# Performance work log

Hardware: AMD Instinct MI355X
Metric: run time of the kernel (lower is better)

Reference implementation:

```python
import math
import jax, jax.numpy as jnp
import numpy as np


def _shapley_tables(L):
    """Static subset-lattice tables for L views.

    masks: [M, L] 0/1 membership of view l in subset m (M = 2^L).
    coef:  [L, M] Shapley combination coefficients so that
           shapley[l] = sum_m coef[l, m] * relu(Linear(sum_{j in m} feats[j])).
    Derivation (faithful to the torch loops): for view i and every nonempty
    subset S not containing i, contrib = f(sum_{S u {i}}) - f(feats_i) with
    weight |S|! (L-|S|-1)! / L!, plus f(feats_i)/L.  Letting T = S u {i}
    (|T| >= 2, i in T) and noting sum of weights over all S is (L-1)/L and
    f(feats_i) = f(sum over singleton {i}):
      coef[i, T]          = (|T|-1)! (L-|T|)! / L!   for |T|>=2, i in T
      coef[i, {i}]       += -(L-1)/L + 1/L = -(L-2)/L
    """
    M = 1 << L
    fact = math.factorial
    masks = np.zeros((M, L), np.float32)
    coef = np.zeros((L, M), np.float32)
    for m in range(M):
        bits = [i for i in range(L) if (m >> i) & 1]
        for i in bits:
            masks[m, i] = 1.0
        t = len(bits)
        if t >= 2:
            wgt = fact(t - 1) * fact(L - t) / fact(L)
            for i in bits:
                coef[i, m] += wgt
    for i in range(L):
        coef[i, 1 << i] += -(L - 2) / L
    return jnp.asarray(masks), jnp.asarray(coef)


def setup_inputs() -> dict:
    key = jax.random.key(0)
    k1, k2 = jax.random.split(key)
    L, C, H, W = 5, 64, 128, 256
    feats = jax.random.normal(k1, (L, C, H, W), dtype=jnp.float32)
    w = jax.random.normal(k2, (C, 1), dtype=jnp.float32) / np.sqrt(C)
    b = jnp.zeros((1,), dtype=jnp.float32)
    return {"feats": feats, "w": w, "b": b}


def reference(feats, w, b):
    L, C, H, W = feats.shape
    N = H * W
    masks, coef = _shapley_tables(L)
    x = feats.reshape(L, C, N).transpose(0, 2, 1)          # [L, N, C]
    # all 2^L subset sums in one GEMM over the (tiny) L axis
    subset_sums = jnp.einsum('ml,lnc->mnc', masks, x)       # [M, N, C]
    f_sums = jax.nn.relu(subset_sums @ w + b)               # [M, N, 1]
    shapley = jnp.einsum('lm,mnj->lnj', coef, f_sums)       # [L, N, 1]
    attn = jax.nn.softmax(shapley, axis=0)                  # softmax over views
    fused = jnp.sum(x * attn, axis=0)                       # [N, C]
    return fused.T.reshape(C, H, W)
```

## Files before the change

### kernel.cpp

```cpp
#include <hip/hip_runtime.h>


constexpr int L_VIEWS = 5;
constexpr int C_CH    = 64;
constexpr int NPIX    = 128 * 256;

typedef float floatx4 __attribute__((ext_vector_type(4)));

__global__ __launch_bounds__(256, 4)
void shapley_fusion_kernel(const float* __restrict__ feats,
                           const float* __restrict__ w,
                           const float* __restrict__ bptr,
                           float* __restrict__ out)
{
    const int tid  = threadIdx.x;
    const int h    = tid >> 6;
    const int lane = tid & 63;
    const int q    = lane & 7;
    const int g    = (lane >> 3) & 7;
    const int win  = blockIdx.x * 32;
    const int nq   = win + q * 4;
    const int cA   = h * 8 + g;
    const int cB   = cA + 32;

    const float w0   = w[cA];
    const float w1   = w[cB];
    const float bias = bptr[0];

    float4 va[L_VIEWS][2];
#pragma unroll
    for (int l = 0; l < L_VIEWS; ++l) {
        va[l][0] = *reinterpret_cast<const float4*>(
            feats + ((size_t)(l * C_CH + cA) * NPIX + nq));
        va[l][1] = *reinterpret_cast<const float4*>(
            feats + ((size_t)(l * C_CH + cB) * NPIX + nq));
    }

    float d[L_VIEWS][4];
#pragma unroll
    for (int l = 0; l < L_VIEWS; ++l) {
        d[l][0] = va[l][0].x * w0 + va[l][1].x * w1;
        d[l][1] = va[l][0].y * w0 + va[l][1].y * w1;
        d[l][2] = va[l][0].z * w0 + va[l][1].z * w1;
        d[l][3] = va[l][0].w * w0 + va[l][1].w * w1;
    }

#pragma unroll
    for (int l = 0; l < L_VIEWS; ++l) {
#pragma unroll
        for (int j = 0; j < 4; ++j) {
            d[l][j] += __shfl_xor(d[l][j], 8, 64);
            d[l][j] += __shfl_xor(d[l][j], 16, 64);
            d[l][j] += __shfl_xor(d[l][j], 32, 64);
        }
    }

    __shared__ float4 xl[4][8][L_VIEWS];
    if (g == 0) {
#pragma unroll
        for (int l = 0; l < L_VIEWS; ++l) {
            float4 t; t.x = d[l][0]; t.y = d[l][1]; t.z = d[l][2]; t.w = d[l][3];
            xl[h][q][l] = t;
        }
    }
    __syncthreads();

    const int jm = g & 3;
    const float* xf = reinterpret_cast<const float*>(xl);
    float dm[L_VIEWS];
#pragma unroll
    for (int l = 0; l < L_VIEWS; ++l) {
        float s = 0.f;
#pragma unroll
        for (int hh = 0; hh < 4; ++hh)
            s += xf[(((hh * 8 + q) * L_VIEWS) + l) * 4 + jm];
        dm[l] = s;
    }

    constexpr float WTS[6] = {0.f, -0.6f, 0.05f, 1.0f / 30.0f, 0.05f, 0.2f};

    float S = bias;
    float sh[L_VIEWS] = {0.f, 0.f, 0.f, 0.f, 0.f};
#pragma unroll
    for (int t = 1; t < 32; ++t) {
        const int gm   = t ^ (t >> 1);
        const int bit  = __builtin_ctz(t);
        const bool add = (gm >> bit) & 1;
        S = add ? (S + dm[bit]) : (S - dm[bit]);
        const float f  = fmaxf(S, 0.f);
        const float wt = WTS[__builtin_popcount(gm)];
#pragma unroll
        for (int i = 0; i < L_VIEWS; ++i)
            if (gm & (1 << i)) sh[i] += wt * f;
    }

    float mx = sh[0];
#pragma unroll
    for (int i = 1; i < L_VIEWS; ++i) mx = fmaxf(mx, sh[i]);
    float e[L_VIEWS];
    float sum = 0.f;
#pragma unroll
    for (int i = 0; i < L_VIEWS; ++i) { e[i] = __expf(sh[i] - mx); sum += e[i]; }
    const float inv = 1.f / sum;
    float attn_mine[L_VIEWS];
#pragma unroll
    for (int i = 0; i < L_VIEWS; ++i) attn_mine[i] = e[i] * inv;

    float attn[L_VIEWS][4];
#pragma unroll
    for (int l = 0; l < L_VIEWS; ++l)
#pragma unroll
        for (int j = 0; j < 4; ++j)
            attn[l][j] = __shfl(attn_mine[l], q + 8 * j, 64);

#pragma unroll
    for (int k = 0; k < 2; ++k) {
        const int c = (k == 0) ? cA : cB;
        floatx4 acc;
        acc.x = va[0][k].x * attn[0][0];
        acc.y = va[0][k].y * attn[0][1];
        acc.z = va[0][k].z * attn[0][2];
        acc.w = va[0][k].w * attn[0][3];
#pragma unroll
        for (int l = 1; l < L_VIEWS; ++l) {
            acc.x += va[l][k].x * attn[l][0];
            acc.y += va[l][k].y * attn[l][1];
            acc.z += va[l][k].z * attn[l][2];
            acc.w += va[l][k].w * attn[l][3];
        }
        __builtin_nontemporal_store(acc,
            reinterpret_cast<floatx4*>(out + (size_t)c * NPIX + nq));
    }
}

extern "C" void kernel_launch(void* const* d_in, const int* in_sizes, int n_in,
                              void* d_out, int out_size, void* d_ws, size_t ws_size,
                              hipStream_t stream) {
    const float* feats = (const float*)d_in[0];
    const float* w     = (const float*)d_in[1];
    const float* b     = (const float*)d_in[2];
    float* out         = (float*)d_out;

    shapley_fusion_kernel<<<NPIX / 32, 256, 0, stream>>>(feats, w, b, out);
}
```

Before: 15.59 us.

## Process two pixel windows per block and use DPP for xor-8 reduction

Each block now handles two 32-pixel windows. Both windows' feature loads are issued up front, so twice the memory traffic is in flight per thread before any compute starts. The first butterfly step of the channel reduction becomes a DPP row operation instead of a ds_swizzle/shuffle. The launch-bounds occupancy hint is dropped and the grid is halved. The cost is doubled register pressure for the loaded data, plus lower occupancy and fewer blocks.

```diff
diff --git a/kernel.cpp b/kernel.cpp
--- a/kernel.cpp
+++ b/kernel.cpp
@@ -7,65 +7,50 @@
 
 typedef float floatx4 __attribute__((ext_vector_type(4)));
 
-__global__ __launch_bounds__(256, 4)
-void shapley_fusion_kernel(const float* __restrict__ feats,
-                           const float* __restrict__ w,
-                           const float* __restrict__ bptr,
-                           float* __restrict__ out)
+__device__ __forceinline__ float xor8_add_dpp(float x) {
+    int y = __builtin_amdgcn_update_dpp(0, __float_as_int(x),
+                                        0x128 , 0xF, 0xF, true);
+    return x + __int_as_float(y);
+}
+
+struct Ctx {
+    int q, g, h, jm, cA, cB;
+    float w0, w1, bias;
+};
+
+__device__ __forceinline__ void window_compute(
+    const Ctx& cx, const float4 (&va)[L_VIEWS][2], int nq,
+    float4 (*xl)[8][L_VIEWS],
+    float* __restrict__ out)
 {
-    const int tid  = threadIdx.x;
-    const int h    = tid >> 6;
-    const int lane = tid & 63;
-    const int q    = lane & 7;
-    const int g    = (lane >> 3) & 7;
-    const int win  = blockIdx.x * 32;
-    const int nq   = win + q * 4;
-    const int cA   = h * 8 + g;
-    const int cB   = cA + 32;
-
-    const float w0   = w[cA];
-    const float w1   = w[cB];
-    const float bias = bptr[0];
-
-    float4 va[L_VIEWS][2];
-#pragma unroll
-    for (int l = 0; l < L_VIEWS; ++l) {
-        va[l][0] = *reinterpret_cast<const float4*>(
-            feats + ((size_t)(l * C_CH + cA) * NPIX + nq));
-        va[l][1] = *reinterpret_cast<const float4*>(
-            feats + ((size_t)(l * C_CH + cB) * NPIX + nq));
-    }
-
     float d[L_VIEWS][4];
 #pragma unroll
     for (int l = 0; l < L_VIEWS; ++l) {
-        d[l][0] = va[l][0].x * w0 + va[l][1].x * w1;
-        d[l][1] = va[l][0].y * w0 + va[l][1].y * w1;
-        d[l][2] = va[l][0].z * w0 + va[l][1].z * w1;
-        d[l][3] = va[l][0].w * w0 + va[l][1].w * w1;
+        d[l][0] = va[l][0].x * cx.w0 + va[l][1].x * cx.w1;
+        d[l][1] = va[l][0].y * cx.w0 + va[l][1].y * cx.w1;
+        d[l][2] = va[l][0].z * cx.w0 + va[l][1].z * cx.w1;
+        d[l][3] = va[l][0].w * cx.w0 + va[l][1].w * cx.w1;
     }
 
 #pragma unroll
     for (int l = 0; l < L_VIEWS; ++l) {
 #pragma unroll
         for (int j = 0; j < 4; ++j) {
-            d[l][j] += __shfl_xor(d[l][j], 8, 64);
+            d[l][j] = xor8_add_dpp(d[l][j]);
             d[l][j] += __shfl_xor(d[l][j], 16, 64);
             d[l][j] += __shfl_xor(d[l][j], 32, 64);
         }
     }
 
-    __shared__ float4 xl[4][8][L_VIEWS];
-    if (g == 0) {
+    if (cx.g == 0) {
 #pragma unroll
         for (int l = 0; l < L_VIEWS; ++l) {
             float4 t; t.x = d[l][0]; t.y = d[l][1]; t.z = d[l][2]; t.w = d[l][3];
-            xl[h][q][l] = t;
+            xl[cx.h][cx.q][l] = t;
         }
     }
     __syncthreads();
 
-    const int jm = g & 3;
     const float* xf = reinterpret_cast<const float*>(xl);
     float dm[L_VIEWS];
 #pragma unroll
@@ -73,13 +58,12 @@
         float s = 0.f;
 #pragma unroll
         for (int hh = 0; hh < 4; ++hh)
-            s += xf[(((hh * 8 + q) * L_VIEWS) + l) * 4 + jm];
+            s += xf[(((hh * 8 + cx.q) * L_VIEWS) + l) * 4 + cx.jm];
         dm[l] = s;
     }
 
     constexpr float WTS[6] = {0.f, -0.6f, 0.05f, 1.0f / 30.0f, 0.05f, 0.2f};
-
-    float S = bias;
+    float S = cx.bias;
     float sh[L_VIEWS] = {0.f, 0.f, 0.f, 0.f, 0.f};
 #pragma unroll
     for (int t = 1; t < 32; ++t) {
@@ -111,11 +95,11 @@
     for (int l = 0; l < L_VIEWS; ++l)
 #pragma unroll
         for (int j = 0; j < 4; ++j)
-            attn[l][j] = __shfl(attn_mine[l], q + 8 * j, 64);
+            attn[l][j] = __shfl(attn_mine[l], cx.q + 8 * j, 64);
 
 #pragma unroll
     for (int k = 0; k < 2; ++k) {
-        const int c = (k == 0) ? cA : cB;
+        const int c = (k == 0) ? cx.cA : cx.cB;
         floatx4 acc;
         acc.x = va[0][k].x * attn[0][0];
         acc.y = va[0][k].y * attn[0][1];
@@ -133,6 +117,50 @@
     }
 }
 
+__global__ __launch_bounds__(256)
+void shapley_fusion_kernel(const float* __restrict__ feats,
+                           const float* __restrict__ w,
+                           const float* __restrict__ bptr,
+                           float* __restrict__ out)
+{
+    Ctx cx;
+    const int tid  = threadIdx.x;
+    cx.h    = tid >> 6;
+    const int lane = tid & 63;
+    cx.q    = lane & 7;
+    cx.g    = (lane >> 3) & 7;
+    cx.jm   = cx.g & 3;
+    cx.cA   = cx.h * 8 + cx.g;
+    cx.cB   = cx.cA + 32;
+    cx.w0   = w[cx.cA];
+    cx.w1   = w[cx.cB];
+    cx.bias = bptr[0];
+
+    const int n0 = blockIdx.x * 64 + cx.q * 4;
+    const int n1 = n0 + 32;
+
+    __shared__ float4 xl[2][4][8][L_VIEWS];
+
+    float4 va0[L_VIEWS][2], va1[L_VIEWS][2];
+#pragma unroll
+    for (int l = 0; l < L_VIEWS; ++l) {
+        va0[l][0] = *reinterpret_cast<const float4*>(
+            feats + ((size_t)(l * C_CH + cx.cA) * NPIX + n0));
+        va0[l][1] = *reinterpret_cast<const float4*>(
+            feats + ((size_t)(l * C_CH + cx.cB) * NPIX + n0));
+    }
+#pragma unroll
+    for (int l = 0; l < L_VIEWS; ++l) {
+        va1[l][0] = *reinterpret_cast<const float4*>(
+            feats + ((size_t)(l * C_CH + cx.cA) * NPIX + n1));
+        va1[l][1] = *reinterpret_cast<const float4*>(
+            feats + ((size_t)(l * C_CH + cx.cB) * NPIX + n1));
+    }
+
+    window_compute(cx, va0, n0, xl[0], out);
+    window_compute(cx, va1, n1, xl[1], out);
+}
+
 extern "C" void kernel_launch(void* const* d_in, const int* in_sizes, int n_in,
                               void* d_out, int out_size, void* d_ws, size_t ws_size,
                               hipStream_t stream) {
@@ -141,5 +169,5 @@
     const float* b     = (const float*)d_in[2];
     float* out         = (float*)d_out;
 
-    shapley_fusion_kernel<<<NPIX / 32, 256, 0, stream>>>(feats, w, b, out);
+    shapley_fusion_kernel<<<NPIX / 64, 256, 0, stream>>>(feats, w, b, out);
 }
```

After: 15.27 us. -2.1%, faster.

## Make kernel persistent with register double-buffered prefetch and transpose-style shuffle reduction

Applied to the files above, without the earlier changes.

Launches a fixed grid of 256 blocks that each loop over several 32-pixel windows, prefetching the next window's features into a second register set while the current one is processed. The channel mapping changes to adjacent channel pairs, and the cross-lane reduction becomes a butterfly transpose that needs fewer shuffles, followed by a double-buffered shared-memory combine across waves. This is meant to hide global load latency and cut shuffle count, but it doubles register usage and reduces the number of resident waves, which may limit memory-level parallelism on a bandwidth-bound kernel.

```diff
diff --git a/kernel.cpp b/kernel.cpp
--- a/kernel.cpp
+++ b/kernel.cpp
@@ -4,10 +4,12 @@
 constexpr int L_VIEWS = 5;
 constexpr int C_CH    = 64;
 constexpr int NPIX    = 128 * 256;
+constexpr int NBLK    = 256;
+constexpr int NITER   = NPIX / (NBLK * 32);
 
 typedef float floatx4 __attribute__((ext_vector_type(4)));
 
-__global__ __launch_bounds__(256, 4)
+__global__ __launch_bounds__(256)
 void shapley_fusion_kernel(const float* __restrict__ feats,
                            const float* __restrict__ w,
                            const float* __restrict__ bptr,
@@ -16,120 +18,145 @@
     const int tid  = threadIdx.x;
     const int h    = tid >> 6;
     const int lane = tid & 63;
-    const int q    = lane & 7;
-    const int g    = (lane >> 3) & 7;
-    const int win  = blockIdx.x * 32;
-    const int nq   = win + q * 4;
-    const int cA   = h * 8 + g;
-    const int cB   = cA + 32;
+    const int n8   = lane & 7;
+    const int cg   = lane >> 3;
+    const int jm   = cg & 3;
+    const int cA   = h * 16 + cg * 2;
+    const int cB   = cA + 1;
 
     const float w0   = w[cA];
     const float w1   = w[cB];
     const float bias = bptr[0];
 
-    float4 va[L_VIEWS][2];
+    __shared__ float xw[2][4][8][8][L_VIEWS];
+
+    float4 vaA[L_VIEWS][2], vaB[L_VIEWS][2];
+
+    {
+        const int nq = (0 * NBLK + blockIdx.x) * 32 + n8 * 4;
 #pragma unroll
-    for (int l = 0; l < L_VIEWS; ++l) {
-        va[l][0] = *reinterpret_cast<const float4*>(
-            feats + ((size_t)(l * C_CH + cA) * NPIX + nq));
-        va[l][1] = *reinterpret_cast<const float4*>(
-            feats + ((size_t)(l * C_CH + cB) * NPIX + nq));
-    }
-
-    float d[L_VIEWS][4];
-#pragma unroll
-    for (int l = 0; l < L_VIEWS; ++l) {
-        d[l][0] = va[l][0].x * w0 + va[l][1].x * w1;
-        d[l][1] = va[l][0].y * w0 + va[l][1].y * w1;
-        d[l][2] = va[l][0].z * w0 + va[l][1].z * w1;
-        d[l][3] = va[l][0].w * w0 + va[l][1].w * w1;
+        for (int l = 0; l < L_VIEWS; ++l) {
+            vaA[l][0] = *reinterpret_cast<const float4*>(
+                feats + ((size_t)(l * C_CH + cA) * NPIX + nq));
+            vaA[l][1] = *reinterpret_cast<const float4*>(
+                feats + ((size_t)(l * C_CH + cB) * NPIX + nq));
+        }
     }
 
 #pragma unroll
-    for (int l = 0; l < L_VIEWS; ++l) {
+    for (int k = 0; k < NITER; ++k) {
+        const bool useA = (k & 1) == 0;
+        const int nq = (k * NBLK + blockIdx.x) * 32 + n8 * 4;
+
+        if (k + 1 < NITER) {
+            const int nq2 = ((k + 1) * NBLK + blockIdx.x) * 32 + n8 * 4;
+            float4 (&vn)[L_VIEWS][2] = useA ? vaB : vaA;
 #pragma unroll
-        for (int j = 0; j < 4; ++j) {
-            d[l][j] += __shfl_xor(d[l][j], 8, 64);
-            d[l][j] += __shfl_xor(d[l][j], 16, 64);
-            d[l][j] += __shfl_xor(d[l][j], 32, 64);
+            for (int l = 0; l < L_VIEWS; ++l) {
+                vn[l][0] = *reinterpret_cast<const float4*>(
+                    feats + ((size_t)(l * C_CH + cA) * NPIX + nq2));
+                vn[l][1] = *reinterpret_cast<const float4*>(
+                    feats + ((size_t)(l * C_CH + cB) * NPIX + nq2));
+            }
         }
-    }
 
-    __shared__ float4 xl[4][8][L_VIEWS];
-    if (g == 0) {
+        const float4 (&va)[L_VIEWS][2] = useA ? vaA : vaB;
+
+        float d[L_VIEWS][4];
 #pragma unroll
         for (int l = 0; l < L_VIEWS; ++l) {
-            float4 t; t.x = d[l][0]; t.y = d[l][1]; t.z = d[l][2]; t.w = d[l][3];
-            xl[h][q][l] = t;
+            d[l][0] = va[l][0].x * w0 + va[l][1].x * w1;
+            d[l][1] = va[l][0].y * w0 + va[l][1].y * w1;
+            d[l][2] = va[l][0].z * w0 + va[l][1].z * w1;
+            d[l][3] = va[l][0].w * w0 + va[l][1].w * w1;
         }
-    }
-    __syncthreads();
 
-    const int jm = g & 3;
-    const float* xf = reinterpret_cast<const float*>(xl);
-    float dm[L_VIEWS];
+        const bool b0 = (cg & 1) != 0;
+        const bool b1 = (cg & 2) != 0;
+        float dd[L_VIEWS];
 #pragma unroll
-    for (int l = 0; l < L_VIEWS; ++l) {
-        float s = 0.f;
+        for (int l = 0; l < L_VIEWS; ++l) {
+            const float s0 = b0 ? d[l][0] : d[l][1];
+            const float r0 = __shfl_xor(s0, 8, 64);
+            const float k0 = (b0 ? d[l][1] : d[l][0]) + r0;
+            const float s1 = b0 ? d[l][2] : d[l][3];
+            const float r1 = __shfl_xor(s1, 8, 64);
+            const float k1 = (b0 ? d[l][3] : d[l][2]) + r1;
+            const float s2 = b1 ? k0 : k1;
+            const float r2 = __shfl_xor(s2, 16, 64);
+            float v = (b1 ? k1 : k0) + r2;
+            v += __shfl_xor(v, 32, 64);
+            dd[l] = v;
+        }
+
+        const int buf = k & 1;
 #pragma unroll
-        for (int hh = 0; hh < 4; ++hh)
-            s += xf[(((hh * 8 + q) * L_VIEWS) + l) * 4 + jm];
-        dm[l] = s;
-    }
+        for (int l = 0; l < L_VIEWS; ++l)
+            xw[buf][h][n8][cg][l] = dd[l];
+        __syncthreads();
 
-    constexpr float WTS[6] = {0.f, -0.6f, 0.05f, 1.0f / 30.0f, 0.05f, 0.2f};
+        float dm[L_VIEWS];
+#pragma unroll
+        for (int l = 0; l < L_VIEWS; ++l) {
+            float s = dd[l];
+#pragma unroll
+            for (int hh = 1; hh < 4; ++hh)
+                s += xw[buf][(h + hh) & 3][n8][cg][l];
+            dm[l] = s;
+        }
 
-    float S = bias;
-    float sh[L_VIEWS] = {0.f, 0.f, 0.f, 0.f, 0.f};
+        constexpr float WTS[6] = {0.f, -0.6f, 0.05f, 1.0f / 30.0f, 0.05f, 0.2f};
+        float S = bias;
+        float sh[L_VIEWS] = {0.f, 0.f, 0.f, 0.f, 0.f};
 #pragma unroll
-    for (int t = 1; t < 32; ++t) {
-        const int gm   = t ^ (t >> 1);
-        const int bit  = __builtin_ctz(t);
-        const bool add = (gm >> bit) & 1;
-        S = add ? (S + dm[bit]) : (S - dm[bit]);
-        const float f  = fmaxf(S, 0.f);
-        const float wt = WTS[__builtin_popcount(gm)];
+        for (int t = 1; t < 32; ++t) {
+            const int gm   = t ^ (t >> 1);
+            const int bit  = __builtin_ctz(t);
+            const bool add = (gm >> bit) & 1;
+            S = add ? (S + dm[bit]) : (S - dm[bit]);
+            const float f  = fmaxf(S, 0.f);
+            const float wt = WTS[__builtin_popcount(gm)];
 #pragma unroll
-        for (int i = 0; i < L_VIEWS; ++i)
-            if (gm & (1 << i)) sh[i] += wt * f;
-    }
+            for (int i = 0; i < L_VIEWS; ++i)
+                if (gm & (1 << i)) sh[i] += wt * f;
+        }
+        float mx = sh[0];
+#pragma unroll
+        for (int i = 1; i < L_VIEWS; ++i) mx = fmaxf(mx, sh[i]);
+        float e[L_VIEWS];
+        float sum = 0.f;
+#pragma unroll
+        for (int i = 0; i < L_VIEWS; ++i) { e[i] = __expf(sh[i] - mx); sum += e[i]; }
+        const float inv = 1.f / sum;
+        float attn_mine[L_VIEWS];
+#pragma unroll
+        for (int i = 0; i < L_VIEWS; ++i) attn_mine[i] = e[i] * inv;
 
-    float mx = sh[0];
+        float attn[L_VIEWS][4];
 #pragma unroll
-    for (int i = 1; i < L_VIEWS; ++i) mx = fmaxf(mx, sh[i]);
-    float e[L_VIEWS];
-    float sum = 0.f;
+        for (int l = 0; l < L_VIEWS; ++l)
 #pragma unroll
-    for (int i = 0; i < L_VIEWS; ++i) { e[i] = __expf(sh[i] - mx); sum += e[i]; }
-    const float inv = 1.f / sum;
-    float attn_mine[L_VIEWS];
-#pragma unroll
-    for (int i = 0; i < L_VIEWS; ++i) attn_mine[i] = e[i] * inv;
-
-    float attn[L_VIEWS][4];
-#pragma unroll
-    for (int l = 0; l < L_VIEWS; ++l)
-#pragma unroll
-        for (int j = 0; j < 4; ++j)
-            attn[l][j] = __shfl(attn_mine[l], q + 8 * j, 64);
+            for (int j = 0; j < 4; ++j)
+                attn[l][j] = __shfl(attn_mine[l], n8 + 8 * (j + (cg & 4)), 64);
 
 #pragma unroll
-    for (int k = 0; k < 2; ++k) {
-        const int c = (k == 0) ? cA : cB;
-        floatx4 acc;
-        acc.x = va[0][k].x * attn[0][0];
-        acc.y = va[0][k].y * attn[0][1];
-        acc.z = va[0][k].z * attn[0][2];
-        acc.w = va[0][k].w * attn[0][3];
+        for (int kk = 0; kk < 2; ++kk) {
+            const int c = (kk == 0) ? cA : cB;
+            floatx4 acc;
+            acc.x = va[0][kk].x * attn[0][0];
+            acc.y = va[0][kk].y * attn[0][1];
+            acc.z = va[0][kk].z * attn[0][2];
+            acc.w = va[0][kk].w * attn[0][3];
 #pragma unroll
-        for (int l = 1; l < L_VIEWS; ++l) {
-            acc.x += va[l][k].x * attn[l][0];
-            acc.y += va[l][k].y * attn[l][1];
-            acc.z += va[l][k].z * attn[l][2];
-            acc.w += va[l][k].w * attn[l][3];
+            for (int l = 1; l < L_VIEWS; ++l) {
+                acc.x += va[l][kk].x * attn[l][0];
+                acc.y += va[l][kk].y * attn[l][1];
+                acc.z += va[l][kk].z * attn[l][2];
+                acc.w += va[l][kk].w * attn[l][3];
+            }
+            __builtin_nontemporal_store(acc,
+                reinterpret_cast<floatx4*>(out + (size_t)c * NPIX + nq));
         }
-        __builtin_nontemporal_store(acc,
-            reinterpret_cast<floatx4*>(out + (size_t)c * NPIX + nq));
     }
 }
 
@@ -141,5 +168,5 @@
     const float* b     = (const float*)d_in[2];
     float* out         = (float*)d_out;
 
-    shapley_fusion_kernel<<<NPIX / 32, 256, 0, stream>>>(feats, w, b, out);
+    shapley_fusion_kernel<<<NBLK, 256, 0, stream>>>(feats, w, b, out);
 }
```

Result: faster. 14.79 us (-5.1%).
